# Kernel optimization log

Measured on AMD Instinct MI355X. Metric: run time of the kernel, lower is better.

The kernel has to match this reference:

```python
import jax, jax.numpy as jnp
import numpy as np

D_MODEL = 512
NUM_HEADS = 8
D_K = D_MODEL // NUM_HEADS


def setup_inputs() -> dict:
    key = jax.random.key(0)
    ks = jax.random.split(key, 11)
    B, S = 2, 4096
    s = 1.0 / np.sqrt(D_MODEL)
    inp = {
        "q": jax.random.normal(ks[0], (B, S, D_MODEL), jnp.float32),
        "k": jax.random.normal(ks[1], (B, S, D_MODEL), jnp.float32),
        "v": jax.random.normal(ks[2], (B, S, D_MODEL), jnp.float32),
        "Wq": jax.random.normal(ks[3], (D_MODEL, D_MODEL), jnp.float32) * s,
        "bq": jnp.zeros((D_MODEL,), jnp.float32),
        "Wk": jax.random.normal(ks[4], (D_MODEL, D_MODEL), jnp.float32) * s,
        "bk": jnp.zeros((D_MODEL,), jnp.float32),
        "Wv": jax.random.normal(ks[5], (D_MODEL, D_MODEL), jnp.float32) * s,
        "bv": jnp.zeros((D_MODEL,), jnp.float32),
        "Wo": jax.random.normal(ks[6], (D_MODEL, D_MODEL), jnp.float32) * s,
        "bo": jnp.zeros((D_MODEL,), jnp.float32),
    }
    return inp


def reference(q, k, v, Wq, bq, Wk, bk, Wv, bv, Wo, bo):
    B, S, _ = q.shape
    # Linear projections (torch Linear: x @ W.T + b)
    def proj(x, W, b):
        y = jnp.einsum("bsd,ed->bse", x, W) + b
        return y.reshape(B, -1, NUM_HEADS, D_K).transpose(0, 2, 1, 3)  # [B,H,S,d_k]

    qh = proj(q, Wq, bq)
    kh = proj(k, Wk, bk)
    vh = proj(v, Wv, bv)

    scale = 1.0 / np.sqrt(D_K).astype(np.float32)
    scores = jnp.einsum("bhqd,bhkd->bhqk", qh, kh) * scale  # [B,H,S,S]
    attn = jax.nn.softmax(scores, axis=-1)
    ctx = jnp.einsum("bhqk,bhkd->bhqd", attn, vh)  # [B,H,S,d_k]
    ctx = ctx.transpose(0, 2, 1, 3).reshape(B, -1, D_MODEL)
    out = jnp.einsum("bsd,ed->bse", ctx, Wo) + bo
    return out
```

## Files before the change

kernel.cpp:

```cpp
#include <hip/hip_runtime.h>
#include <hip/hip_bf16.h>
#include <stdint.h>


typedef float  floatx4 __attribute__((ext_vector_type(4)));
typedef __bf16 bf16x8  __attribute__((ext_vector_type(8)));
typedef short  shortx4 __attribute__((ext_vector_type(4)));

#define MFMA16(a, b, c) __builtin_amdgcn_mfma_f32_16x16x32_bf16((a), (b), (c), 0, 0, 0)

#define QSCALE 0.1803368801111244f

__device__ __forceinline__ short f2bf(float f) {
  union { float f; uint32_t u; } a; a.f = f;
  uint32_t u = a.u;
  u += 0x7fffu + ((u >> 16) & 1u);
  return (short)(u >> 16);
}

__device__ __forceinline__ void stage16(const short* g, short* l) {
  __builtin_amdgcn_global_load_lds(
      (const __attribute__((address_space(1))) void*)g,
      (__attribute__((address_space(3))) void*)l, 16, 0, 0);
}

__global__ __launch_bounds__(256) void cvt3_kernel(const float* __restrict__ q,
                                                   const float* __restrict__ k,
                                                   const float* __restrict__ v,
                                                   short* __restrict__ out, int n4) {
  const int which = blockIdx.y;
  const float* in = which == 0 ? q : which == 1 ? k : v;
  short* o = out + (size_t)which * (size_t)n4 * 4;
  int i = blockIdx.x * 256 + threadIdx.x;
  if (i < n4) {
    float4 f = reinterpret_cast<const float4*>(in)[i];
    shortx4 s;
    s.x = f2bf(f.x); s.y = f2bf(f.y); s.z = f2bf(f.z); s.w = f2bf(f.w);
    reinterpret_cast<shortx4*>(o)[i] = s;
  }
}

__global__ __launch_bounds__(256) void cvtw_kernel(const float* __restrict__ w0,
                                                   const float* __restrict__ w1,
                                                   const float* __restrict__ w2,
                                                   const float* __restrict__ w3,
                                                   short* __restrict__ out, int n4) {
  const int which = blockIdx.y;
  const float* in = which == 0 ? w0 : which == 1 ? w1 : which == 2 ? w2 : w3;
  short* o = out + (size_t)which * (size_t)n4 * 4;
  int i = blockIdx.x * 256 + threadIdx.x;
  if (i < n4) {
    float4 f = reinterpret_cast<const float4*>(in)[i];
    shortx4 s;
    s.x = f2bf(f.x); s.y = f2bf(f.y); s.z = f2bf(f.z); s.w = f2bf(f.w);
    reinterpret_cast<shortx4*>(o)[i] = s;
  }
}

__global__ __launch_bounds__(256) void proj3_kernel(
    const short* __restrict__ xq, const short* __restrict__ xk, const short* __restrict__ xv,
    const short* __restrict__ wq, const short* __restrict__ wk, const short* __restrict__ wv,
    const float* __restrict__ bq, const float* __restrict__ bk, const float* __restrict__ bv,
    short* __restrict__ Qh, short* __restrict__ KV) {
  const int which = blockIdx.z;
  const short* A = which == 0 ? xq : which == 1 ? xk : xv;
  const short* W = which == 0 ? wq : which == 1 ? wk : wv;
  const float* bias = which == 0 ? bq : which == 1 ? bk : bv;

  __shared__ __align__(16) short sA[2][4096];
  __shared__ __align__(16) short sB[2][2048];

  const int K = 512;
  const int tid = threadIdx.x;
  const int lane = tid & 63;
  const int wave = tid >> 6;
  const int l15 = lane & 15;
  const int quad = lane >> 4;
  const int tileM = blockIdx.x * 128;
  const int tileN = blockIdx.y * 64;

  const int srow = tid >> 2;
  const int fr = (srow ^ (srow >> 2)) & 3;
  const int sq = ((tid & 3) ^ fr) * 8;
  const short* As0 = A + (size_t)(tileM + srow) * K + sq;
  const short* As1 = As0 + (size_t)64 * K;
  const short* Bs  = W + (size_t)(tileN + srow) * K + sq;
  const int ldw = wave * 512;

  const int fl = (l15 ^ (l15 >> 2)) & 3;
  const int qsw = (quad ^ fl) * 8;
  const int ra0 = (wave * 32 + l15) * 32 + qsw;
  const int ra1 = ra0 + 512;
  const int rb0 = l15 * 32 + qsw;

  floatx4 acc[2][4];
#pragma unroll
  for (int mt = 0; mt < 2; ++mt)
#pragma unroll
    for (int nt = 0; nt < 4; ++nt) acc[mt][nt] = (floatx4){0.f, 0.f, 0.f, 0.f};

  stage16(As0, &sA[0][ldw]);
  stage16(As1, &sA[0][2048 + ldw]);
  stage16(Bs,  &sB[0][ldw]);

#pragma unroll 2
  for (int t = 0; t < 16; ++t) {
    __syncthreads();
    if (t != 15) {
      const int kk = (t + 1) * 32;
      short* a_ld = &sA[(t + 1) & 1][ldw];
      stage16(As0 + kk, a_ld);
      stage16(As1 + kk, a_ld + 2048);
      stage16(Bs + kk, &sB[(t + 1) & 1][ldw]);
    }
    const short* sa = sA[t & 1];
    const short* sb = sB[t & 1];
    bf16x8 a0 = *(const bf16x8*)&sa[ra0];
    bf16x8 a1 = *(const bf16x8*)&sa[ra1];
#pragma unroll
    for (int nt = 0; nt < 4; ++nt) {
      bf16x8 wf = *(const bf16x8*)&sb[rb0 + nt * 512];
      acc[0][nt] = MFMA16(a0, wf, acc[0][nt]);
      acc[1][nt] = MFMA16(a1, wf, acc[1][nt]);
    }
  }

#pragma unroll
  for (int mt = 0; mt < 2; ++mt) {
    const int rowbase = tileM + wave * 32 + mt * 16 + quad * 4;
    const int b = rowbase >> 12, s = rowbase & 4095;
    const int g = s >> 5;
    if (which == 0) {
#pragma unroll
      for (int nt = 0; nt < 4; ++nt) {
        const int col = tileN + nt * 16 + l15;
        const int h = col >> 6, d = col & 63;
        const float bc = bias[col];
#pragma unroll
        for (int r = 0; r < 4; ++r) {
          const int row = rowbase + r;
          const int ss = row & 4095;
          Qh[(size_t)((b * 8 + h) * 4096 + ss) * 64 + d] = f2bf((acc[mt][nt][r] + bc) * QSCALE);
        }
      }
    } else if (which == 1) {
      const int key = s & 31;
      const int t = key >> 4;
      const int l15b = key & 15;
#pragma unroll
      for (int nt = 0; nt < 4; ++nt) {
        const int col = tileN + nt * 16 + l15;
        const int h = col >> 6, dd = col & 63;
        const int ks = dd >> 5, quadk = (dd >> 3) & 3, jj = dd & 7;
        const float bc = bias[col];
        const size_t base = ((size_t)(b * 8 + h) * 128 + g) * 4096 +
                            (size_t)(t * 2 + ks) * 512 + (size_t)quadk * 128 + jj;
#pragma unroll
        for (int r = 0; r < 4; ++r)
          KV[base + (size_t)(l15b + r) * 8] = f2bf(acc[mt][nt][r] + bc);
      }
    } else {
      const int p32 = s & 31;
      const int l0 = ((p32 & 15) >> 2) * 8 + (p32 >> 4) * 4;
      const int quadv = l0 >> 3, jv = l0 & 7;
#pragma unroll
      for (int nt = 0; nt < 4; ++nt) {
        const int col = tileN + nt * 16 + l15;
        const int h = col >> 6, dd = col & 63;
        const int dt = dd >> 4, l15v = dd & 15;
        const float bc = bias[col];
        shortx4 p;
        p.x = f2bf(acc[mt][nt][0] + bc);
        p.y = f2bf(acc[mt][nt][1] + bc);
        p.z = f2bf(acc[mt][nt][2] + bc);
        p.w = f2bf(acc[mt][nt][3] + bc);
        *(shortx4*)(KV + ((size_t)(b * 8 + h) * 128 + g) * 4096 + 2048 +
                    (size_t)dt * 512 + (size_t)quadv * 128 + (size_t)l15v * 8 + jv) = p;
      }
    }
  }
}

__global__ __launch_bounds__(256) void proj_o_kernel(
    const short* __restrict__ A, const short* __restrict__ W,
    const float* __restrict__ bias, float* __restrict__ out) {
  __shared__ __align__(16) short sA[2][4096];
  __shared__ __align__(16) short sB[2][2048];

  const int K = 512;
  const int tid = threadIdx.x;
  const int lane = tid & 63;
  const int wave = tid >> 6;
  const int l15 = lane & 15;
  const int quad = lane >> 4;
  const int tileM = blockIdx.x * 128;
  const int tileN = blockIdx.y * 64;

  const int srow = tid >> 2;
  const int fr = (srow ^ (srow >> 2)) & 3;
  const int sq = ((tid & 3) ^ fr) * 8;
  const short* As0 = A + (size_t)(tileM + srow) * K + sq;
  const short* As1 = As0 + (size_t)64 * K;
  const short* Bs  = W + (size_t)(tileN + srow) * K + sq;
  const int ldw = wave * 512;

  const int fl = (l15 ^ (l15 >> 2)) & 3;
  const int qsw = (quad ^ fl) * 8;
  const int ra0 = (wave * 32 + l15) * 32 + qsw;
  const int ra1 = ra0 + 512;
  const int rb0 = l15 * 32 + qsw;

  floatx4 acc[2][4];
#pragma unroll
  for (int mt = 0; mt < 2; ++mt)
#pragma unroll
    for (int nt = 0; nt < 4; ++nt) acc[mt][nt] = (floatx4){0.f, 0.f, 0.f, 0.f};

  stage16(As0, &sA[0][ldw]);
  stage16(As1, &sA[0][2048 + ldw]);
  stage16(Bs,  &sB[0][ldw]);

#pragma unroll 2
  for (int t = 0; t < 16; ++t) {
    __syncthreads();
    if (t != 15) {
      const int kk = (t + 1) * 32;
      short* a_ld = &sA[(t + 1) & 1][ldw];
      stage16(As0 + kk, a_ld);
      stage16(As1 + kk, a_ld + 2048);
      stage16(Bs + kk, &sB[(t + 1) & 1][ldw]);
    }
    const short* sa = sA[t & 1];
    const short* sb = sB[t & 1];
    bf16x8 a0 = *(const bf16x8*)&sa[ra0];
    bf16x8 a1 = *(const bf16x8*)&sa[ra1];
#pragma unroll
    for (int nt = 0; nt < 4; ++nt) {
      bf16x8 wf = *(const bf16x8*)&sb[rb0 + nt * 512];
      acc[0][nt] = MFMA16(a0, wf, acc[0][nt]);
      acc[1][nt] = MFMA16(a1, wf, acc[1][nt]);
    }
  }

#pragma unroll
  for (int mt = 0; mt < 2; ++mt) {
    const int rowbase = tileM + wave * 32 + mt * 16 + quad * 4;
#pragma unroll
    for (int nt = 0; nt < 4; ++nt) {
      const int col = tileN + nt * 16 + l15;
      const float bc = bias[col];
#pragma unroll
      for (int r = 0; r < 4; ++r) out[(size_t)(rowbase + r) * 512 + col] = acc[mt][nt][r] + bc;
    }
  }
}

__global__ __launch_bounds__(512) void flash_kernel(
    const short* __restrict__ Qh, const short* __restrict__ KV,
    short* __restrict__ ctx) {
  __shared__ __align__(16) short sKV[2][8192];
  __shared__ float comb[4][64][34];

  const int id = blockIdx.x;
  const int xcd = id & 7;
  const int j = id >> 3;
  const int bh = xcd + ((j >> 5) << 3);
  const int qtile = j & 31;

  const int tid = threadIdx.x;
  const int wave = tid >> 6;
  const int lane = tid & 63;
  const int l15 = lane & 15;
  const int quad = lane >> 4;
  const int wq = wave & 3;
  const int half = wave >> 2;
  const int qrow0 = qtile * 128 + wq * 32;

  bf16x8 qf[2][2];
#pragma unroll
  for (int nt = 0; nt < 2; ++nt) {
    const short* Qb = Qh + (size_t)(bh * 4096 + qrow0 + nt * 16 + l15) * 64 + quad * 8;
    qf[nt][0] = *(const bf16x8*)(Qb);
    qf[nt][1] = *(const bf16x8*)(Qb + 32);
  }

  bf16x8 ones;
  {
    union { short s[8]; bf16x8 v; } u;
#pragma unroll
    for (int i = 0; i < 8; ++i) u.s[i] = (short)0x3F80;
    ones = u.v;
  }

  const short* KVb = KV + (size_t)bh * (128 * 4096);
  const short* sg = KVb + wave * 512 + lane * 8;
  const int ldw = wave * 512;

  const floatx4 FZ = (floatx4){0.f, 0.f, 0.f, 0.f};
  floatx4 o[2][4];
  floatx4 lacc[2];
#pragma unroll
  for (int nt = 0; nt < 2; ++nt) {
    lacc[nt] = FZ;
#pragma unroll
    for (int dt = 0; dt < 4; ++dt) o[nt][dt] = FZ;
  }

  stage16(sg, &sKV[0][ldw]);
  stage16(sg + 4096, &sKV[0][ldw + 4096]);

#define COMPUTE(S) do {                                                         \
    bf16x8 ka[2][2], vf[4];                                                     \
    ka[0][0] = *(const bf16x8*)&(S)[av];                                        \
    ka[0][1] = *(const bf16x8*)&(S)[av + 512];                                  \
    ka[1][0] = *(const bf16x8*)&(S)[av + 1024];                                 \
    ka[1][1] = *(const bf16x8*)&(S)[av + 1536];                                 \
    vf[0] = *(const bf16x8*)&(S)[av + 2048];                                    \
    vf[1] = *(const bf16x8*)&(S)[av + 2560];                                    \
    vf[2] = *(const bf16x8*)&(S)[av + 3072];                                    \
    vf[3] = *(const bf16x8*)&(S)[av + 3584];                                    \
    floatx4 st[2][2];                                                           \
    _Pragma("unroll")                                                           \
    for (int nt = 0; nt < 2; ++nt)                                              \
      _Pragma("unroll")                                                         \
      for (int t = 0; t < 2; ++t)                                               \
        st[nt][t] = MFMA16(ka[t][1], qf[nt][1], MFMA16(ka[t][0], qf[nt][0], FZ)); \
    bf16x8 pb[2];                                                               \
    _Pragma("unroll")                                                           \
    for (int nt = 0; nt < 2; ++nt) {                                            \
      float p[8];                                                               \
      _Pragma("unroll")                                                         \
      for (int t = 0; t < 2; ++t)                                               \
        _Pragma("unroll")                                                       \
        for (int r = 0; r < 4; ++r) p[t * 4 + r] = __builtin_amdgcn_exp2f(st[nt][t][r]); \
      union { __hip_bfloat162 h2[4]; bf16x8 v8; } u;                            \
      u.h2[0] = __float22bfloat162_rn(float2{p[0], p[1]});                      \
      u.h2[1] = __float22bfloat162_rn(float2{p[2], p[3]});                      \
      u.h2[2] = __float22bfloat162_rn(float2{p[4], p[5]});                      \
      u.h2[3] = __float22bfloat162_rn(float2{p[6], p[7]});                      \
      pb[nt] = u.v8;                                                            \
    }                                                                           \
    _Pragma("unroll")                                                           \
    for (int nt = 0; nt < 2; ++nt) {                                            \
      lacc[nt] = MFMA16(ones, pb[nt], lacc[nt]);                                \
      _Pragma("unroll")                                                         \
      for (int dt = 0; dt < 4; ++dt)                                            \
        o[nt][dt] = MFMA16(vf[dt], pb[nt], o[nt][dt]);                          \
    }                                                                           \
  } while (0)

  const int av = lane * 8;

  for (int it = 0; it < 64; ++it) {
    __syncthreads();

    if (it != 63) {
      const short* gs = sg + (size_t)(2 * it + 2) * 4096;
      short* ld = &sKV[(it + 1) & 1][ldw];
      stage16(gs, ld);
      stage16(gs + 4096, ld + 4096);
    }

    const short* S = sKV[it & 1] + (half << 12);
    COMPUTE(S);
  }
#undef COMPUTE

  __syncthreads();
  if (half) {
    float* cb = comb[wq][lane];
#pragma unroll
    for (int nt = 0; nt < 2; ++nt) {
#pragma unroll
      for (int dt = 0; dt < 4; ++dt)
#pragma unroll
        for (int r = 0; r < 4; ++r) cb[nt * 16 + dt * 4 + r] = o[nt][dt][r];
      cb[32 + nt] = lacc[nt][0];
    }
  }
  __syncthreads();
  if (!half) {
    const float* cb = comb[wq][lane];
    const int b = bh >> 3, h = bh & 7;
#pragma unroll
    for (int nt = 0; nt < 2; ++nt) {
      const float inv = 1.0f / (lacc[nt][0] + cb[32 + nt]);
      const int row = qrow0 + nt * 16 + l15;
      short* cp = ctx + (size_t)(b * 4096 + row) * 512 + h * 64 + quad * 4;
#pragma unroll
      for (int dt = 0; dt < 4; ++dt) {
        union { __hip_bfloat162 h2[2]; shortx4 s4; } u;
        u.h2[0] = __float22bfloat162_rn(
            float2{(o[nt][dt][0] + cb[nt * 16 + dt * 4 + 0]) * inv,
                   (o[nt][dt][1] + cb[nt * 16 + dt * 4 + 1]) * inv});
        u.h2[1] = __float22bfloat162_rn(
            float2{(o[nt][dt][2] + cb[nt * 16 + dt * 4 + 2]) * inv,
                   (o[nt][dt][3] + cb[nt * 16 + dt * 4 + 3]) * inv});
        *(shortx4*)(cp + dt * 16) = u.s4;
      }
    }
  }
}

extern "C" void kernel_launch(void* const* d_in, const int* in_sizes, int n_in,
                              void* d_out, int out_size, void* d_ws, size_t ws_size,
                              hipStream_t stream) {
  const float* q  = (const float*)d_in[0];
  const float* k  = (const float*)d_in[1];
  const float* v  = (const float*)d_in[2];
  const float* Wq = (const float*)d_in[3];
  const float* bq = (const float*)d_in[4];
  const float* Wk = (const float*)d_in[5];
  const float* bk = (const float*)d_in[6];
  const float* Wv = (const float*)d_in[7];
  const float* bv = (const float*)d_in[8];
  const float* Wo = (const float*)d_in[9];
  const float* bo = (const float*)d_in[10];

  const int XN = 2 * 4096 * 512;
  const int WN = 512 * 512;

  short* ws  = (short*)d_ws;
  short* xqb = ws;
  short* xkb = ws + (size_t)XN;
  short* xvb = ws + (size_t)2 * XN;
  short* wqb = ws + (size_t)3 * XN;
  short* wkb = wqb + WN;
  short* wvb = wkb + WN;
  short* wob = wvb + WN;
  short* Qh  = wob + WN;
  short* KVf = Qh + (size_t)XN;
  short* ctx = xqb;

  dim3 cg(XN / 4 / 256, 3);
  cvt3_kernel<<<cg, 256, 0, stream>>>(q, k, v, xqb, XN / 4);
  dim3 wg(WN / 4 / 256, 4);
  cvtw_kernel<<<wg, 256, 0, stream>>>(Wq, Wk, Wv, Wo, wqb, WN / 4);

  dim3 pg(64, 8, 3);
  proj3_kernel<<<pg, 256, 0, stream>>>(xqb, xkb, xvb, wqb, wkb, wvb,
                                       bq, bk, bv, Qh, KVf);

  flash_kernel<<<512, 512, 0, stream>>>(Qh, KVf, ctx);

  dim3 og(64, 8);
  proj_o_kernel<<<og, 256, 0, stream>>>(ctx, wob, bo, (float*)d_out);
}
```

Before: 212.7 us.

## Software-pipeline flash loop with triple-buffered LDS and V tiles shifted by one block

Changes the flash attention loop so that the QK MFMAs for the next KV block run while the exp/pack and PV MFMAs for the previous block are processed. The projection kernel now writes V tiles one slot ahead (slot g+2 mod 128), so each staged tile pairs K of block i with V of block i-1; the leftover V block is staged again and consumed after the loop. LDS becomes a 3-deep ring with explicit vmcnt waits and raw s_barrier, s_setprio is raised around compute, and the combine buffer now reuses the sKV memory. This is meant to hide exp latency and global-to-LDS load latency behind MFMA work, at the cost of more registers and a tighter coupling between the KV layout and the loop schedule.

```diff
diff --git a/kernel.cpp b/kernel.cpp
--- a/kernel.cpp
+++ b/kernel.cpp
@@ -145,7 +145,7 @@
       }
     } else if (which == 1) {
       const int key = s & 31;
-      const int t = key >> 4;
+      const int tt = key >> 4;
       const int l15b = key & 15;
 #pragma unroll
       for (int nt = 0; nt < 4; ++nt) {
@@ -154,12 +154,13 @@
         const int ks = dd >> 5, quadk = (dd >> 3) & 3, jj = dd & 7;
         const float bc = bias[col];
         const size_t base = ((size_t)(b * 8 + h) * 128 + g) * 4096 +
-                            (size_t)(t * 2 + ks) * 512 + (size_t)quadk * 128 + jj;
+                            (size_t)(tt * 2 + ks) * 512 + (size_t)quadk * 128 + jj;
 #pragma unroll
         for (int r = 0; r < 4; ++r)
           KV[base + (size_t)(l15b + r) * 8] = f2bf(acc[mt][nt][r] + bc);
       }
     } else {
+      const int slot = (g + 2) & 127;
       const int p32 = s & 31;
       const int l0 = ((p32 & 15) >> 2) * 8 + (p32 >> 4) * 4;
       const int quadv = l0 >> 3, jv = l0 & 7;
@@ -174,7 +175,7 @@
         p.y = f2bf(acc[mt][nt][1] + bc);
         p.z = f2bf(acc[mt][nt][2] + bc);
         p.w = f2bf(acc[mt][nt][3] + bc);
-        *(shortx4*)(KV + ((size_t)(b * 8 + h) * 128 + g) * 4096 + 2048 +
+        *(shortx4*)(KV + ((size_t)(b * 8 + h) * 128 + slot) * 4096 + 2048 +
                     (size_t)dt * 512 + (size_t)quadv * 128 + (size_t)l15v * 8 + jv) = p;
       }
     }
@@ -258,8 +259,7 @@
 __global__ __launch_bounds__(512) void flash_kernel(
     const short* __restrict__ Qh, const short* __restrict__ KV,
     short* __restrict__ ctx) {
-  __shared__ __align__(16) short sKV[2][8192];
-  __shared__ float comb[4][64][34];
+  __shared__ __align__(16) short sKV[3][8192];
 
   const int id = blockIdx.x;
   const int xcd = id & 7;
@@ -295,6 +295,7 @@
   const short* KVb = KV + (size_t)bh * (128 * 4096);
   const short* sg = KVb + wave * 512 + lane * 8;
   const int ldw = wave * 512;
+  const int av = lane * 8;
 
   const floatx4 FZ = (floatx4){0.f, 0.f, 0.f, 0.f};
   floatx4 o[2][4];
@@ -306,96 +307,176 @@
     for (int dt = 0; dt < 4; ++dt) o[nt][dt] = FZ;
   }
 
+  floatx4 stA[2][2], stB[2][2];
+
   stage16(sg, &sKV[0][ldw]);
   stage16(sg + 4096, &sKV[0][ldw + 4096]);
-
-#define COMPUTE(S) do {                                                         \
-    bf16x8 ka[2][2], vf[4];                                                     \
-    ka[0][0] = *(const bf16x8*)&(S)[av];                                        \
-    ka[0][1] = *(const bf16x8*)&(S)[av + 512];                                  \
-    ka[1][0] = *(const bf16x8*)&(S)[av + 1024];                                 \
-    ka[1][1] = *(const bf16x8*)&(S)[av + 1536];                                 \
-    vf[0] = *(const bf16x8*)&(S)[av + 2048];                                    \
-    vf[1] = *(const bf16x8*)&(S)[av + 2560];                                    \
-    vf[2] = *(const bf16x8*)&(S)[av + 3072];                                    \
-    vf[3] = *(const bf16x8*)&(S)[av + 3584];                                    \
-    floatx4 st[2][2];                                                           \
-    _Pragma("unroll")                                                           \
-    for (int nt = 0; nt < 2; ++nt)                                              \
-      _Pragma("unroll")                                                         \
-      for (int t = 0; t < 2; ++t)                                               \
-        st[nt][t] = MFMA16(ka[t][1], qf[nt][1], MFMA16(ka[t][0], qf[nt][0], FZ)); \
-    bf16x8 pb[2];                                                               \
-    _Pragma("unroll")                                                           \
-    for (int nt = 0; nt < 2; ++nt) {                                            \
-      float p[8];                                                               \
-      _Pragma("unroll")                                                         \
-      for (int t = 0; t < 2; ++t)                                               \
-        _Pragma("unroll")                                                       \
-        for (int r = 0; r < 4; ++r) p[t * 4 + r] = __builtin_amdgcn_exp2f(st[nt][t][r]); \
-      union { __hip_bfloat162 h2[4]; bf16x8 v8; } u;                            \
-      u.h2[0] = __float22bfloat162_rn(float2{p[0], p[1]});                      \
-      u.h2[1] = __float22bfloat162_rn(float2{p[2], p[3]});                      \
-      u.h2[2] = __float22bfloat162_rn(float2{p[4], p[5]});                      \
-      u.h2[3] = __float22bfloat162_rn(float2{p[6], p[7]});                      \
-      pb[nt] = u.v8;                                                            \
-    }                                                                           \
-    _Pragma("unroll")                                                           \
-    for (int nt = 0; nt < 2; ++nt) {                                            \
-      lacc[nt] = MFMA16(ones, pb[nt], lacc[nt]);                                \
-      _Pragma("unroll")                                                         \
-      for (int dt = 0; dt < 4; ++dt)                                            \
-        o[nt][dt] = MFMA16(vf[dt], pb[nt], o[nt][dt]);                          \
-    }                                                                           \
-  } while (0)
-
-  const int av = lane * 8;
-
-  for (int it = 0; it < 64; ++it) {
-    __syncthreads();
-
-    if (it != 63) {
-      const short* gs = sg + (size_t)(2 * it + 2) * 4096;
-      short* ld = &sKV[(it + 1) & 1][ldw];
-      stage16(gs, ld);
-      stage16(gs + 4096, ld + 4096);
-    }
-
-    const short* S = sKV[it & 1] + (half << 12);
-    COMPUTE(S);
-  }
-#undef COMPUTE
+  stage16(sg + 8192, &sKV[1][ldw]);
+  stage16(sg + 12288, &sKV[1][ldw + 4096]);
+
+  short* p0 = sKV[0];
+  short* p1 = sKV[1];
+  short* p2 = sKV[2];
+
+#define SYNC_STAGE(IT, LASTWAIT)                                               \
+    if (LASTWAIT) asm volatile("s_waitcnt vmcnt(0) lgkmcnt(0)" ::: "memory");  \
+    else          asm volatile("s_waitcnt vmcnt(2) lgkmcnt(0)" ::: "memory");  \
+    __builtin_amdgcn_s_barrier();                                              \
+    if ((IT) < 62) {                                                           \
+      const short* gs = sg + (size_t)((IT) + 2) * 8192;                        \
+      stage16(gs, p2 + ldw);                                                   \
+      stage16(gs + 4096, p2 + ldw + 4096);                                     \
+    }
+
+#define READS                                                                  \
+    const short* S = p0 + (half << 12);                                        \
+    bf16x8 ka[2][2], vf[4];                                                    \
+    ka[0][0] = *(const bf16x8*)&S[av];                                         \
+    ka[0][1] = *(const bf16x8*)&S[av + 512];                                   \
+    ka[1][0] = *(const bf16x8*)&S[av + 1024];                                  \
+    ka[1][1] = *(const bf16x8*)&S[av + 1536];                                  \
+    vf[0] = *(const bf16x8*)&S[av + 2048];                                     \
+    vf[1] = *(const bf16x8*)&S[av + 2560];                                     \
+    vf[2] = *(const bf16x8*)&S[av + 3072];                                     \
+    vf[3] = *(const bf16x8*)&S[av + 3584];
+
+#define EXPPACK(STP, PB)                                                       \
+    bf16x8 PB[2];                                                              \
+    _Pragma("unroll")                                                          \
+    for (int nt = 0; nt < 2; ++nt) {                                           \
+      float pp[8];                                                             \
+      _Pragma("unroll")                                                        \
+      for (int t = 0; t < 2; ++t)                                              \
+        _Pragma("unroll")                                                      \
+        for (int r = 0; r < 4; ++r)                                            \
+          pp[t * 4 + r] = __builtin_amdgcn_exp2f(STP[nt][t][r]);               \
+      union { __hip_bfloat162 h2[4]; bf16x8 v8; } u;                           \
+      u.h2[0] = __float22bfloat162_rn(float2{pp[0], pp[1]});                   \
+      u.h2[1] = __float22bfloat162_rn(float2{pp[2], pp[3]});                   \
+      u.h2[2] = __float22bfloat162_rn(float2{pp[4], pp[5]});                   \
+      u.h2[3] = __float22bfloat162_rn(float2{pp[6], pp[7]});                   \
+      PB[nt] = u.v8;                                                           \
+    }
+
+#define QK(STC)                                                                \
+    _Pragma("unroll")                                                          \
+    for (int nt = 0; nt < 2; ++nt)                                             \
+      _Pragma("unroll")                                                        \
+      for (int t = 0; t < 2; ++t)                                              \
+        STC[nt][t] = MFMA16(ka[t][1], qf[nt][1], MFMA16(ka[t][0], qf[nt][0], FZ));
+
+#define PV(PB)                                                                 \
+    _Pragma("unroll")                                                          \
+    for (int nt = 0; nt < 2; ++nt) {                                           \
+      lacc[nt] = MFMA16(ones, PB[nt], lacc[nt]);                               \
+      _Pragma("unroll")                                                        \
+      for (int dt = 0; dt < 4; ++dt)                                           \
+        o[nt][dt] = MFMA16(vf[dt], PB[nt], o[nt][dt]);                         \
+    }
+
+#define ROT { short* tr = p0; p0 = p1; p1 = p2; p2 = tr; }
+
+  {
+    SYNC_STAGE(0, false)
+    __builtin_amdgcn_s_setprio(1);
+    READS
+    QK(stA)
+    __builtin_amdgcn_s_setprio(0);
+    ROT
+  }
+
+  for (int p = 0; p < 31; ++p) {
+    const int itO = 1 + 2 * p;
+    {
+      SYNC_STAGE(itO, false)
+      __builtin_amdgcn_s_setprio(1);
+      READS
+      EXPPACK(stA, pbO)
+      QK(stB)
+      PV(pbO)
+      __builtin_amdgcn_s_setprio(0);
+      ROT
+    }
+    {
+      SYNC_STAGE(itO + 1, false)
+      __builtin_amdgcn_s_setprio(1);
+      READS
+      EXPPACK(stB, pbE)
+      QK(stA)
+      PV(pbE)
+      __builtin_amdgcn_s_setprio(0);
+      ROT
+    }
+  }
+
+  {
+    SYNC_STAGE(63, true)
+    __builtin_amdgcn_s_setprio(1);
+    READS
+    EXPPACK(stA, pbL)
+    QK(stB)
+    PV(pbL)
+    __builtin_amdgcn_s_setprio(0);
+  }
+
+  asm volatile("s_waitcnt lgkmcnt(0)" ::: "memory");
+  __builtin_amdgcn_s_barrier();
+  {
+    const short* ge = KVb + (size_t)(wave >> 2) * 4096 + 2048 +
+                      (size_t)(wave & 3) * 512 + lane * 8;
+    stage16(ge, &sKV[0][ldw]);
+  }
+  asm volatile("s_waitcnt vmcnt(0)" ::: "memory");
+  __builtin_amdgcn_s_barrier();
+  {
+    const short* Sv = &sKV[0][half << 11];
+    bf16x8 vf[4];
+    vf[0] = *(const bf16x8*)&Sv[av];
+    vf[1] = *(const bf16x8*)&Sv[av + 512];
+    vf[2] = *(const bf16x8*)&Sv[av + 1024];
+    vf[3] = *(const bf16x8*)&Sv[av + 1536];
+    EXPPACK(stB, pbF)
+    PV(pbF)
+  }
+
+#undef SYNC_STAGE
+#undef READS
+#undef EXPPACK
+#undef QK
+#undef PV
+#undef ROT
 
   __syncthreads();
+  float* cb = (float*)sKV;
   if (half) {
-    float* cb = comb[wq][lane];
+    float* c = cb + (size_t)(wq * 64 + lane) * 34;
 #pragma unroll
     for (int nt = 0; nt < 2; ++nt) {
 #pragma unroll
       for (int dt = 0; dt < 4; ++dt)
 #pragma unroll
-        for (int r = 0; r < 4; ++r) cb[nt * 16 + dt * 4 + r] = o[nt][dt][r];
-      cb[32 + nt] = lacc[nt][0];
+        for (int r = 0; r < 4; ++r) c[nt * 16 + dt * 4 + r] = o[nt][dt][r];
+      c[32 + nt] = lacc[nt][0];
     }
   }
   __syncthreads();
   if (!half) {
-    const float* cb = comb[wq][lane];
+    const float* c = cb + (size_t)(wq * 64 + lane) * 34;
     const int b = bh >> 3, h = bh & 7;
 #pragma unroll
     for (int nt = 0; nt < 2; ++nt) {
-      const float inv = 1.0f / (lacc[nt][0] + cb[32 + nt]);
+      const float inv = 1.0f / (lacc[nt][0] + c[32 + nt]);
       const int row = qrow0 + nt * 16 + l15;
       short* cp = ctx + (size_t)(b * 4096 + row) * 512 + h * 64 + quad * 4;
 #pragma unroll
       for (int dt = 0; dt < 4; ++dt) {
         union { __hip_bfloat162 h2[2]; shortx4 s4; } u;
         u.h2[0] = __float22bfloat162_rn(
-            float2{(o[nt][dt][0] + cb[nt * 16 + dt * 4 + 0]) * inv,
-                   (o[nt][dt][1] + cb[nt * 16 + dt * 4 + 1]) * inv});
+            float2{(o[nt][dt][0] + c[nt * 16 + dt * 4 + 0]) * inv,
+                   (o[nt][dt][1] + c[nt * 16 + dt * 4 + 1]) * inv});
         u.h2[1] = __float22bfloat162_rn(
-            float2{(o[nt][dt][2] + cb[nt * 16 + dt * 4 + 2]) * inv,
-                   (o[nt][dt][3] + cb[nt * 16 + dt * 4 + 3]) * inv});
+            float2{(o[nt][dt][2] + c[nt * 16 + dt * 4 + 2]) * inv,
+                   (o[nt][dt][3] + c[nt * 16 + dt * 4 + 3]) * inv});
         *(shortx4*)(cp + dt * 16) = u.s4;
       }
     }
```

Result: slower. 220.8 us (+3.8%).

## Stage two KV tiles per barrier and reuse KV LDS for combine

Applied to the files above, without the earlier changes.

The flash attention loop now processes two 4096-key chunks per iteration with a four-buffer LDS ring, halving the number of barriers. It uses an explicit waitcnt plus s_barrier, raises wave priority during compute, and reuses the KV shared buffer for the final cross-half combine instead of a separate array. The intent is to cut synchronization overhead and hide load latency better. In exchange LDS use per block roughly doubles for KV, which may lower occupancy.

```diff
diff --git a/kernel.cpp b/kernel.cpp
--- a/kernel.cpp
+++ b/kernel.cpp
@@ -145,7 +145,7 @@
       }
     } else if (which == 1) {
       const int key = s & 31;
-      const int t = key >> 4;
+      const int tt = key >> 4;
       const int l15b = key & 15;
 #pragma unroll
       for (int nt = 0; nt < 4; ++nt) {
@@ -154,7 +154,7 @@
         const int ks = dd >> 5, quadk = (dd >> 3) & 3, jj = dd & 7;
         const float bc = bias[col];
         const size_t base = ((size_t)(b * 8 + h) * 128 + g) * 4096 +
-                            (size_t)(t * 2 + ks) * 512 + (size_t)quadk * 128 + jj;
+                            (size_t)(tt * 2 + ks) * 512 + (size_t)quadk * 128 + jj;
 #pragma unroll
         for (int r = 0; r < 4; ++r)
           KV[base + (size_t)(l15b + r) * 8] = f2bf(acc[mt][nt][r] + bc);
@@ -258,8 +258,7 @@
 __global__ __launch_bounds__(512) void flash_kernel(
     const short* __restrict__ Qh, const short* __restrict__ KV,
     short* __restrict__ ctx) {
-  __shared__ __align__(16) short sKV[2][8192];
-  __shared__ float comb[4][64][34];
+  __shared__ __align__(16) short sKV[4][8192];
 
   const int id = blockIdx.x;
   const int xcd = id & 7;
@@ -295,6 +294,7 @@
   const short* KVb = KV + (size_t)bh * (128 * 4096);
   const short* sg = KVb + wave * 512 + lane * 8;
   const int ldw = wave * 512;
+  const int av = lane * 8;
 
   const floatx4 FZ = (floatx4){0.f, 0.f, 0.f, 0.f};
   floatx4 o[2][4];
@@ -308,6 +308,8 @@
 
   stage16(sg, &sKV[0][ldw]);
   stage16(sg + 4096, &sKV[0][ldw + 4096]);
+  stage16(sg + 8192, &sKV[1][ldw]);
+  stage16(sg + 12288, &sKV[1][ldw + 4096]);
 
 #define COMPUTE(S) do {                                                         \
     bf16x8 ka[2][2], vf[4];                                                     \
@@ -328,16 +330,16 @@
     bf16x8 pb[2];                                                               \
     _Pragma("unroll")                                                           \
     for (int nt = 0; nt < 2; ++nt) {                                            \
-      float p[8];                                                               \
+      float pp[8];                                                              \
       _Pragma("unroll")                                                         \
       for (int t = 0; t < 2; ++t)                                               \
         _Pragma("unroll")                                                       \
-        for (int r = 0; r < 4; ++r) p[t * 4 + r] = __builtin_amdgcn_exp2f(st[nt][t][r]); \
+        for (int r = 0; r < 4; ++r) pp[t * 4 + r] = __builtin_amdgcn_exp2f(st[nt][t][r]); \
       union { __hip_bfloat162 h2[4]; bf16x8 v8; } u;                            \
-      u.h2[0] = __float22bfloat162_rn(float2{p[0], p[1]});                      \
-      u.h2[1] = __float22bfloat162_rn(float2{p[2], p[3]});                      \
-      u.h2[2] = __float22bfloat162_rn(float2{p[4], p[5]});                      \
-      u.h2[3] = __float22bfloat162_rn(float2{p[6], p[7]});                      \
+      u.h2[0] = __float22bfloat162_rn(float2{pp[0], pp[1]});                    \
+      u.h2[1] = __float22bfloat162_rn(float2{pp[2], pp[3]});                    \
+      u.h2[2] = __float22bfloat162_rn(float2{pp[4], pp[5]});                    \
+      u.h2[3] = __float22bfloat162_rn(float2{pp[6], pp[7]});                    \
       pb[nt] = u.v8;                                                            \
     }                                                                           \
     _Pragma("unroll")                                                           \
@@ -349,53 +351,63 @@
     }                                                                           \
   } while (0)
 
-  const int av = lane * 8;
-
-  for (int it = 0; it < 64; ++it) {
-    __syncthreads();
-
-    if (it != 63) {
-      const short* gs = sg + (size_t)(2 * it + 2) * 4096;
-      short* ld = &sKV[(it + 1) & 1][ldw];
-      stage16(gs, ld);
-      stage16(gs + 4096, ld + 4096);
-    }
-
-    const short* S = sKV[it & 1] + (half << 12);
-    COMPUTE(S);
+  short* c0 = sKV[0]; short* c1 = sKV[1];
+  short* n0 = sKV[2]; short* n1 = sKV[3];
+
+  for (int s = 0; s < 32; ++s) {
+    asm volatile("s_waitcnt vmcnt(0) lgkmcnt(0)" ::: "memory");
+    __builtin_amdgcn_s_barrier();
+
+    if (s < 31) {
+      const short* gs = sg + (size_t)(s + 1) * 16384;
+      stage16(gs, n0 + ldw);
+      stage16(gs + 4096, n0 + ldw + 4096);
+      stage16(gs + 8192, n1 + ldw);
+      stage16(gs + 12288, n1 + ldw + 4096);
+    }
+
+    __builtin_amdgcn_s_setprio(1);
+    { const short* S = c0 + (half << 12); COMPUTE(S); }
+    { const short* S = c1 + (half << 12); COMPUTE(S); }
+    __builtin_amdgcn_s_setprio(0);
+
+    short* t;
+    t = c0; c0 = n0; n0 = t;
+    t = c1; c1 = n1; n1 = t;
   }
 #undef COMPUTE
 
   __syncthreads();
+  float* cb = (float*)sKV;
   if (half) {
-    float* cb = comb[wq][lane];
+    float* c = cb + (size_t)(wq * 64 + lane) * 34;
 #pragma unroll
     for (int nt = 0; nt < 2; ++nt) {
 #pragma unroll
       for (int dt = 0; dt < 4; ++dt)
 #pragma unroll
-        for (int r = 0; r < 4; ++r) cb[nt * 16 + dt * 4 + r] = o[nt][dt][r];
-      cb[32 + nt] = lacc[nt][0];
+        for (int r = 0; r < 4; ++r) c[nt * 16 + dt * 4 + r] = o[nt][dt][r];
+      c[32 + nt] = lacc[nt][0];
     }
   }
   __syncthreads();
   if (!half) {
-    const float* cb = comb[wq][lane];
+    const float* c = cb + (size_t)(wq * 64 + lane) * 34;
     const int b = bh >> 3, h = bh & 7;
 #pragma unroll
     for (int nt = 0; nt < 2; ++nt) {
-      const float inv = 1.0f / (lacc[nt][0] + cb[32 + nt]);
+      const float inv = 1.0f / (lacc[nt][0] + c[32 + nt]);
       const int row = qrow0 + nt * 16 + l15;
       short* cp = ctx + (size_t)(b * 4096 + row) * 512 + h * 64 + quad * 4;
 #pragma unroll
       for (int dt = 0; dt < 4; ++dt) {
         union { __hip_bfloat162 h2[2]; shortx4 s4; } u;
         u.h2[0] = __float22bfloat162_rn(
-            float2{(o[nt][dt][0] + cb[nt * 16 + dt * 4 + 0]) * inv,
-                   (o[nt][dt][1] + cb[nt * 16 + dt * 4 + 1]) * inv});
+            float2{(o[nt][dt][0] + c[nt * 16 + dt * 4 + 0]) * inv,
+                   (o[nt][dt][1] + c[nt * 16 + dt * 4 + 1]) * inv});
         u.h2[1] = __float22bfloat162_rn(
-            float2{(o[nt][dt][2] + cb[nt * 16 + dt * 4 + 2]) * inv,
-                   (o[nt][dt][3] + cb[nt * 16 + dt * 4 + 3]) * inv});
+            float2{(o[nt][dt][2] + c[nt * 16 + dt * 4 + 2]) * inv,
+                   (o[nt][dt][3] + c[nt * 16 + dt * 4 + 3]) * inv});
         *(shortx4*)(cp + dt * 16) = u.s4;
       }
     }
```

Measured after the change: 215.9 us. No clear change (+1.5%).
